# Performance work log

Hardware: AMD Instinct MI355X
Metric: run time of the kernel (lower is better)

Reference implementation:

```python
import jax, jax.numpy as jnp
import numpy as np

# ---- db6 filter bank (pywt conventions) ----
_REC_LO = np.array([0.11154074335008017, 0.4946238903983854, 0.7511339080215775,
                    0.3152503517092432, -0.22626469396516913, -0.12976686756709563,
                    0.09750160558707936, 0.02752286553001629, -0.031582039318031156,
                    0.0005538422009938016, 0.004777257511010651, -0.00107730108499558],
                   dtype=np.float32)
_REC_HI = _REC_LO[::-1].copy(); _REC_HI[1::2] *= -1.0          # qmf(rec_lo)
_DEC_LO = _REC_LO[::-1].copy()
_DEC_HI = _REC_HI[::-1].copy()
L = 12          # filter length
LEVEL = 8       # J
# pytorch_wavelets cross-correlates with dec[::-1] == true conv with dec.
# lax.conv_general_dilated is correlation, so analysis kernels = dec[::-1] = rec filters.
ANA = jnp.asarray(np.stack([_REC_LO, _REC_HI])[:, None, :])     # [2,1,L]
SYN = jnp.asarray(np.stack([_DEC_LO, _DEC_HI])[None, :, :])     # [1,2,L]


def dwt1d(x, J):
    """Multi-level DWT, mode='symmetric'. x: [B,C,N] -> (yl [B,C,m], [yh1..yhJ])."""
    B, C, N = x.shape
    lo = x.reshape(B * C, 1, N)
    highs = []
    for _ in range(J):
        n = lo.shape[-1]
        outlen = (n + L - 1) // 2                    # pywt dwt_coeff_len
        p = 2 * (outlen - 1) - n + L
        xp = jnp.pad(lo, ((0, 0), (0, 0), (p // 2, (p + 1) // 2)), mode='symmetric')
        y = jax.lax.conv_general_dilated(xp, ANA, (2,), 'VALID',
                                         dimension_numbers=('NCH', 'OIH', 'NCH'))
        lo = y[:, :1]
        highs.append(y[:, 1:].reshape(B, C, outlen))
    return lo.reshape(B, C, -1), highs


def idwt1d(yl, yhs):
    """Inverse of dwt1d. yl: [B,C,m], yhs list (level1..levelJ)."""
    B, C, _ = yl.shape
    lo = yl.reshape(B * C, 1, -1)
    pad = L - 1 - (L - 2)                            # torch convT padding L-2 -> lax pad 1
    for h in yhs[::-1]:
        h = h.reshape(B * C, 1, -1)
        if lo.shape[-1] > h.shape[-1]:               # 'unpad' extra sample
            lo = lo[..., :h.shape[-1]]
        xh = jnp.concatenate([lo, h], axis=1)        # [BC,2,n]
        lo = jax.lax.conv_general_dilated(xh, SYN, (1,), [(pad, pad)],
                                          lhs_dilation=(2,),
                                          dimension_numbers=('NCH', 'OIH', 'NCH'))
    return lo.reshape(B, C, -1)


def wno_forward(x, fc0_w, fc0_b, w1, w2, cw, cb, fc1_w, fc1_b, fc2_w, fc2_b):
    B, s, _ = x.shape
    grid = jnp.broadcast_to(jnp.linspace(0.0, 1.0, s, dtype=x.dtype)[None, :, None], (B, s, 1))
    v = jnp.concatenate([x, grid], axis=-1) @ fc0_w + fc0_b     # [B,s,W]
    v = v.transpose(0, 2, 1)                                     # [B,W,s]
    n_layers = w1.shape[0]
    for i in range(n_layers):
        yl, yhs = dwt1d(v, LEVEL)
        yl = jnp.einsum('bix,iox->box', yl, w1[i])               # mix approx coeffs
        yhs[-1] = jnp.einsum('bix,iox->box', yhs[-1], w2[i])     # mix finest-level detail
        x1 = idwt1d(yl, yhs)
        x2 = jnp.einsum('bis,io->bos', v, cw[i]) + cb[i][None, :, None]  # 1x1 conv
        v = x1 + x2
        if i < n_layers - 1:
            v = jax.nn.gelu(v, approximate=False)
    v = v.transpose(0, 2, 1)
    v = jax.nn.gelu(v @ fc1_w + fc1_b, approximate=False)
    return v @ fc2_w + fc2_b                                     # [B,s,1]


def setup_inputs() -> dict:
    key = jax.random.key(0)
    B, S, W, NL = 32, 8192, 64, 4
    n = S
    for _ in range(LEVEL):
        n = (n + L - 1) // 2
    modes = n                                                    # 42
    ks = jax.random.split(key, 12)
    scale = 1.0 / (W * W)
    return {
        'x': jax.random.normal(ks[0], (B, S, 1), jnp.float32),
        'fc0_w': jax.random.normal(ks[1], (2, W), jnp.float32) * 0.5,
        'fc0_b': jax.random.normal(ks[2], (W,), jnp.float32) * 0.1,
        'w1': scale * jax.random.uniform(ks[3], (NL, W, W, modes), jnp.float32),
        'w2': scale * jax.random.uniform(ks[4], (NL, W, W, modes), jnp.float32),
        'cw': jax.random.normal(ks[5], (NL, W, W), jnp.float32) * (1.0 / np.sqrt(W)),
        'cb': jax.random.normal(ks[6], (NL, W), jnp.float32) * 0.05,
        'fc1_w': jax.random.normal(ks[7], (W, 128), jnp.float32) * (1.0 / np.sqrt(W)),
        'fc1_b': jax.random.normal(ks[8], (128,), jnp.float32) * 0.05,
        'fc2_w': jax.random.normal(ks[9], (128, 1), jnp.float32) * (1.0 / np.sqrt(128.0)),
        'fc2_b': jax.random.normal(ks[10], (1,), jnp.float32) * 0.05,
    }


def reference(x, fc0_w, fc0_b, w1, w2, cw, cb, fc1_w, fc1_b, fc2_w, fc2_b):
    return wno_forward(x, fc0_w, fc0_b, w1, w2, cw, cb, fc1_w, fc1_b, fc2_w, fc2_b)
```

## Files before the change

### kernel.cpp

```cpp
#include <hip/hip_runtime.h>
#include <cmath>

#define BC 2048
#define S_LEN 8192
#define MODES 42
#define HTOT 8232

static constexpr float C_LO[12] = {
  0.11154074335008017f, 0.4946238903983854f, 0.7511339080215775f,
  0.3152503517092432f, -0.22626469396516913f, -0.12976686756709563f,
  0.09750160558707936f, 0.02752286553001629f, -0.031582039318031156f,
  0.0005538422009938016f, 0.004777257511010651f, -0.00107730108499558f };

__device__ __forceinline__ float rec_lo_c(int k){ return C_LO[k]; }
__device__ __forceinline__ float rec_hi_c(int k){ float v = C_LO[11-k]; return (k&1)? -v : v; }
__device__ __forceinline__ float dec_lo_c(int k){ return C_LO[11-k]; }
__device__ __forceinline__ float dec_hi_c(int k){ float v = C_LO[k];    return (k&1)?  v : -v; }

__device__ __forceinline__ float erf_fast(float x){
  float ax = fabsf(x);
  float t  = __fdividef(1.0f, 1.0f + 0.3275911f * ax);
  float p  = ((((1.061405429f * t - 1.453152027f) * t) + 1.421413741f) * t - 0.284496736f) * t + 0.254829592f;
  float y  = 1.0f - p * t * __expf(-ax * ax);
  return copysignf(y, x);
}
__device__ __forceinline__ float gelu_f(float x){
  return 0.5f * x * (1.0f + erf_fast(x * 0.70710678118654752440f));
}

__device__ __forceinline__ int reflect_i(int t, int n){
  t = (t < 0) ? (-1 - t) : t;
  t = (t >= n) ? (2 * n - 1 - t) : t;
  return t;
}

__device__ __forceinline__ unsigned short bf16_rn(float x){
  unsigned int b = __float_as_uint(x);
  b += 0x7FFF + ((b >> 16) & 1);
  return (unsigned short)(b >> 16);
}
__device__ __forceinline__ float bf16_to_f(unsigned short h){
  return __uint_as_float(((unsigned int)h) << 16);
}

typedef short  v8s __attribute__((ext_vector_type(8)));
typedef float  v4f __attribute__((ext_vector_type(4)));
typedef unsigned short u16;

__global__ __launch_bounds__(256) void prep_split(
    const float* __restrict__ fc1w, const float* __restrict__ cw,
    u16* __restrict__ whH, u16* __restrict__ whL,
    u16* __restrict__ wcH, u16* __restrict__ wcL)
{
  int i = blockIdx.x * 256 + threadIdx.x;
  if (i < 8192) {
    int c = i >> 7, j = i & 127;
    float wv = fc1w[i];
    u16 h = bf16_rn(wv);
    float lo = wv - bf16_to_f(h);
    int cs = c ^ ((j & 7) << 3);
    whH[j * 64 + cs] = h; whL[j * 64 + cs] = bf16_rn(lo);
  }
  int k = i - 8192;
  if (k >= 0 && k < 16384) {
    int l = k >> 12, r = k & 4095;
    int c = r >> 6, o = r & 63;
    float wv = cw[k];
    u16 h = bf16_rn(wv);
    float lo = wv - bf16_to_f(h);
    int cs = c ^ ((o & 7) << 3);
    wcH[l * 4096 + o * 64 + cs] = h; wcL[l * 4096 + o * 64 + cs] = bf16_rn(lo);
  }
}

__global__ __launch_bounds__(256) void fc0_kernel(
    const float* __restrict__ x, const float* __restrict__ w,
    const float* __restrict__ bias, float* __restrict__ v)
{
  int p = blockIdx.x * 256 + threadIdx.x;
  int b = p >> 13, s = p & 8191;
  float xv = x[p];
  float g  = (float)s * (1.0f / 8191.0f);
  for (int c = 0; c < 64; ++c) {
    v[((size_t)(b * 64 + c)) * S_LEN + s] = xv * w[c] + g * w[64 + c] + bias[c];
  }
}

__global__ __launch_bounds__(256) void dwt_big(
    const float* __restrict__ vin, float* __restrict__ highs, float* __restrict__ lo_f)
{
  __shared__ float sV[2184], sL1[1088], sL2[544];
  int seq = blockIdx.x >> 2, c = blockIdx.x & 3;
  const float* src = vin + (size_t)seq * S_LEN;
  float* hseq = highs + (size_t)seq * HTOT;

  int V0 = 2080 * c - 70;
  for (int i = threadIdx.x; i < 2178; i += 256)
    sV[i] = src[reflect_i(V0 + i, 8192)];
  __syncthreads();

  int base1 = 1040 * c - 30;
  for (int u = threadIdx.x; u < 1082; u += 256) {
    int m1 = base1 + u;
    float alo = 0.f, ahi = 0.f;
    #pragma unroll
    for (int k = 0; k < 12; ++k) {
      float x = sV[2 * m1 + k - 10 - V0];
      alo += x * rec_lo_c(k); ahi += x * rec_hi_c(k);
    }
    sL1[u] = alo;
    if (m1 >= 1040 * c && m1 < 1040 * c + 1040 && m1 >= 0 && m1 < 4101) hseq[m1] = ahi;
  }
  __syncthreads();

  int base2 = 520 * c - 10;
  for (int u = threadIdx.x; u < 534; u += 256) {
    int m2 = base2 + u;
    float alo = 0.f, ahi = 0.f;
    #pragma unroll
    for (int k = 0; k < 12; ++k) {
      int t = reflect_i(2 * m2 + k - 10, 4101);
      float x = sL1[t - base1];
      alo += x * rec_lo_c(k); ahi += x * rec_hi_c(k);
    }
    sL2[u] = alo;
    if (m2 >= 520 * c && m2 < 520 * c + 520 && m2 >= 0 && m2 < 2056) hseq[4101 + m2] = ahi;
  }
  __syncthreads();

  for (int u = threadIdx.x; u < 260; u += 256) {
    int m3 = 260 * c + u;
    if (m3 < 1033) {
      float alo = 0.f, ahi = 0.f;
      #pragma unroll
      for (int k = 0; k < 12; ++k) {
        int t = reflect_i(2 * m3 + k - 10, 2056);
        float x = sL2[t - base2];
        alo += x * rec_lo_c(k); ahi += x * rec_hi_c(k);
      }
      lo_f[(size_t)seq * 1033 + m3] = alo;
      hseq[6157 + m3] = ahi;
    }
  }
}

__device__ __forceinline__ void dwt_lvl(const float* in, int n, float* out, int outn, float* hg)
{
  for (int m = threadIdx.x; m < outn; m += 256) {
    float alo = 0.f, ahi = 0.f;
    #pragma unroll
    for (int k = 0; k < 12; ++k) {
      float x = in[reflect_i(2 * m + k - 10, n)];
      alo += x * rec_lo_c(k); ahi += x * rec_hi_c(k);
    }
    out[m] = alo; hg[m] = ahi;
  }
  __syncthreads();
}

__global__ __launch_bounds__(256) void dwt_small(
    const float* __restrict__ lo_f, float* __restrict__ highs, float* __restrict__ yl)
{
  __shared__ float A[1040], Bb[528];
  int seq = blockIdx.x;
  const float* src = lo_f + (size_t)seq * 1033;
  float* hseq = highs + (size_t)seq * HTOT;
  for (int i = threadIdx.x; i < 1033; i += 256) A[i] = src[i];
  __syncthreads();
  dwt_lvl(A, 1033, Bb, 522, hseq + 7190);
  dwt_lvl(Bb, 522, A, 266, hseq + 7712);
  dwt_lvl(A, 266, Bb, 138, hseq + 7978);
  dwt_lvl(Bb, 138, A, 74, hseq + 8116);
  dwt_lvl(A, 74, Bb, 42, hseq + 8190);
  for (int m = threadIdx.x; m < MODES; m += 256) yl[seq * MODES + m] = Bb[m];
}

__global__ __launch_bounds__(256) void mix2(
    const float* __restrict__ yl_raw, const float* __restrict__ highs,
    const float* __restrict__ w1i, const float* __restrict__ w2i,
    float* __restrict__ yl_m, float* __restrict__ yh_m)
{
  bool hi = blockIdx.x >= 336;
  int idx = (blockIdx.x - (hi ? 336 : 0)) * 256 + threadIdx.x;
  if (idx >= 32 * 64 * MODES) return;
  int xx = idx % MODES;
  int o  = (idx / MODES) % 64;
  int b  = idx / (MODES * 64);
  const float* in = hi ? (highs + 8190) : yl_raw;
  size_t stride   = hi ? HTOT : MODES;
  const float* w  = hi ? w2i : w1i;
  float acc = 0.f;
  for (int i = 0; i < 64; ++i)
    acc += in[((size_t)(b * 64 + i)) * stride + xx] * w[(i * 64 + o) * MODES + xx];
  (hi ? yh_m : yl_m)[(b * 64 + o) * MODES + xx] = acc;
}

__device__ __forceinline__ void idwt_lvl(const float* lo, const float* h, float* out, int outn)
{
  const int par = threadIdx.x & 1;
  for (int m = threadIdx.x; m < outn; m += 256) {
    int t0 = (m - par) >> 1;
    float acc = 0.f;
    #pragma unroll
    for (int i = 0; i < 6; ++i) {
      float cl = par ? dec_lo_c(2 * i) : dec_lo_c(2 * i + 1);
      float ch = par ? dec_hi_c(2 * i) : dec_hi_c(2 * i + 1);
      acc += lo[t0 + i] * cl + h[t0 + i] * ch;
    }
    out[m] = acc;
  }
}

__device__ __forceinline__ void stage_band(float* dst, const float* src, int len, int alloc)
{
  for (int i = threadIdx.x; i < alloc; i += 256) dst[i] = (i < len) ? src[i] : 0.f;
}

__global__ __launch_bounds__(256) void idwt_small(
    const float* __restrict__ yl_m, const float* __restrict__ yh_m,
    const float* __restrict__ highs, float* __restrict__ lo_i)
{
  __shared__ float bands[1132];
  __shared__ float wa[1040], wb[528];
  int seq = blockIdx.x;
  const float* hseq = highs + (size_t)seq * HTOT;
  stage_band(bands + 0,   yl_m + (size_t)seq * MODES, 42, 50);
  stage_band(bands + 50,  yh_m + (size_t)seq * MODES, 42, 50);
  stage_band(bands + 100, hseq + 8116, 74, 82);
  stage_band(bands + 182, hseq + 7978, 138, 146);
  stage_band(bands + 328, hseq + 7712, 266, 274);
  stage_band(bands + 602, hseq + 7190, 522, 530);
  __syncthreads();
  idwt_lvl(bands + 0, bands + 50, wa, 74);    __syncthreads();
  idwt_lvl(wa, bands + 100, wb, 138);         __syncthreads();
  idwt_lvl(wb, bands + 182, wa, 266);         __syncthreads();
  idwt_lvl(wa, bands + 328, wb, 522);         __syncthreads();
  const int par = threadIdx.x & 1;
  for (int m = threadIdx.x; m < 1033; m += 256) {
    int t0 = (m - par) >> 1;
    float acc = 0.f;
    #pragma unroll
    for (int i = 0; i < 6; ++i) {
      float cl = par ? dec_lo_c(2 * i) : dec_lo_c(2 * i + 1);
      float ch = par ? dec_hi_c(2 * i) : dec_hi_c(2 * i + 1);
      acc += wb[t0 + i] * cl + bands[602 + t0 + i] * ch;
    }
    lo_i[(size_t)seq * 1033 + m] = acc;
  }
}

__global__ __launch_bounds__(256) void idwt_big(
    const float* __restrict__ lo_i, const float* __restrict__ highs, float* __restrict__ x1)
{
  __shared__ float sL3[280], sH3[280], sL2[544], sH2[544], sL1[1040], sH1[1040];
  int seq = blockIdx.x >> 2, c = blockIdx.x & 3;
  const float* hseq = highs + (size_t)seq * HTOT;
  const float* l3   = lo_i + (size_t)seq * 1033;
  int b3 = 256 * c - 2, b2 = 512 * c - 2, b1 = 1024 * c - 2;
  const int par = threadIdx.x & 1;

  for (int i = threadIdx.x; i < 280; i += 256) {
    int g = b3 + i;
    bool ok = (g >= 0 && g < 1033);
    sL3[i] = ok ? l3[g] : 0.f;
    sH3[i] = ok ? hseq[6157 + g] : 0.f;
  }
  for (int i = threadIdx.x; i < 536; i += 256) {
    int g = b2 + i;
    sH2[i] = (g >= 0 && g < 2056) ? hseq[4101 + g] : 0.f;
  }
  for (int i = threadIdx.x; i < 1040; i += 256) {
    int g = b1 + i;
    sH1[i] = (g >= 0 && g < 4101) ? hseq[g] : 0.f;
  }
  __syncthreads();

  for (int u = threadIdx.x; u < 536; u += 256) {
    int m = b2 + u;
    int t0 = ((m - par) >> 1) - b3;
    float acc = 0.f;
    #pragma unroll
    for (int i = 0; i < 6; ++i) {
      float cl = par ? dec_lo_c(2 * i) : dec_lo_c(2 * i + 1);
      float ch = par ? dec_hi_c(2 * i) : dec_hi_c(2 * i + 1);
      acc += sL3[t0 + i] * cl + sH3[t0 + i] * ch;
    }
    sL2[u] = (m >= 0 && m < 2056) ? acc : 0.f;
  }
  __syncthreads();

  for (int u = threadIdx.x; u < 1040; u += 256) {
    int m = b1 + u;
    int t0 = ((m - par) >> 1) - b2;
    float acc = 0.f;
    #pragma unroll
    for (int i = 0; i < 6; ++i) {
      float cl = par ? dec_lo_c(2 * i) : dec_lo_c(2 * i + 1);
      float ch = par ? dec_hi_c(2 * i) : dec_hi_c(2 * i + 1);
      acc += sL2[t0 + i] * cl + sH2[t0 + i] * ch;
    }
    sL1[u] = (m >= 0 && m < 4101) ? acc : 0.f;
  }
  __syncthreads();

  for (int u = threadIdx.x; u < 2048; u += 256) {
    int m = 2048 * c + u;
    int t0 = ((m - par) >> 1) - b1;
    float acc = 0.f;
    #pragma unroll
    for (int i = 0; i < 6; ++i) {
      float cl = par ? dec_lo_c(2 * i) : dec_lo_c(2 * i + 1);
      float ch = par ? dec_hi_c(2 * i) : dec_hi_c(2 * i + 1);
      acc += sL1[t0 + i] * cl + sH1[t0 + i] * ch;
    }
    x1[(size_t)seq * S_LEN + m] = acc;
  }
}

__global__ __launch_bounds__(256) void pw_mfma(
    const float* __restrict__ x1, float* v,
    const u16* __restrict__ wcH, const u16* __restrict__ wcL,
    const float* __restrict__ cb, int do_gelu)
{
  __shared__ u16 aH[64][64], aL[64][64];
  __shared__ u16 wH[64][64], wL[64][64];
  __shared__ float cbl[64];
  int b  = blockIdx.x >> 7;
  int s0 = (blockIdx.x & 127) << 6;
  int t  = threadIdx.x;

  {
    const v8s* srcH = (const v8s*)wcH;
    const v8s* srcL = (const v8s*)wcL;
    v8s* dstH = (v8s*)&wH[0][0];
    v8s* dstL = (v8s*)&wL[0][0];
    #pragma unroll
    for (int r = 0; r < 2; ++r) {
      dstH[t + 256 * r] = srcH[t + 256 * r];
      dstL[t + 256 * r] = srcL[t + 256 * r];
    }
  }
  if (t < 64) cbl[t] = cb[t];

  #pragma unroll
  for (int r = 0; r < 4; ++r) {
    int idx = t + 256 * r;
    int ch = idx >> 4, p4 = (idx & 15) << 2;
    float4 xv = *(const float4*)&v[((size_t)(b * 64 + ch)) * S_LEN + s0 + p4];
    u16 h0 = bf16_rn(xv.x); aH[p4+0][ch ^ (((p4+0)&7)<<3)] = h0; aL[p4+0][ch ^ (((p4+0)&7)<<3)] = bf16_rn(xv.x - bf16_to_f(h0));
    u16 h1 = bf16_rn(xv.y); aH[p4+1][ch ^ (((p4+1)&7)<<3)] = h1; aL[p4+1][ch ^ (((p4+1)&7)<<3)] = bf16_rn(xv.y - bf16_to_f(h1));
    u16 h2 = bf16_rn(xv.z); aH[p4+2][ch ^ (((p4+2)&7)<<3)] = h2; aL[p4+2][ch ^ (((p4+2)&7)<<3)] = bf16_rn(xv.z - bf16_to_f(h2));
    u16 h3 = bf16_rn(xv.w); aH[p4+3][ch ^ (((p4+3)&7)<<3)] = h3; aL[p4+3][ch ^ (((p4+3)&7)<<3)] = bf16_rn(xv.w - bf16_to_f(h3));
  }
  __syncthreads();

  int l = t & 63, wv_ = t >> 6;
  int pi = l & 15, kg = l >> 4;
  int pos = wv_ * 16 + pi;
  int swz = (pi & 7) << 3;

  v4f acc[4];
  #pragma unroll
  for (int i = 0; i < 4; ++i) acc[i] = v4f{0.f, 0.f, 0.f, 0.f};

  #pragma unroll
  for (int kt = 0; kt < 2; ++kt) {
    int ka = (kg * 8 + kt * 32) ^ swz;
    v8s ah = *(const v8s*)&aH[pos][ka];
    v8s al = *(const v8s*)&aL[pos][ka];
    #pragma unroll
    for (int ct = 0; ct < 4; ++ct) {
      int o = ct * 16 + pi;
      v8s bh = *(const v8s*)&wH[o][ka];
      v8s bl = *(const v8s*)&wL[o][ka];
      acc[ct] = __builtin_amdgcn_mfma_f32_16x16x32_bf16(ah, bh, acc[ct], 0, 0, 0);
      acc[ct] = __builtin_amdgcn_mfma_f32_16x16x32_bf16(ah, bl, acc[ct], 0, 0, 0);
      acc[ct] = __builtin_amdgcn_mfma_f32_16x16x32_bf16(al, bh, acc[ct], 0, 0, 0);
    }
  }

  #pragma unroll
  for (int ct = 0; ct < 4; ++ct) {
    int o = ct * 16 + pi;
    size_t base = ((size_t)(b * 64 + o)) * S_LEN + s0 + wv_ * 16 + kg * 4;
    float4 x4 = *(const float4*)&x1[base];
    float cbv = cbl[o];
    float y0 = acc[ct][0] + x4.x + cbv;
    float y1 = acc[ct][1] + x4.y + cbv;
    float y2 = acc[ct][2] + x4.z + cbv;
    float y3 = acc[ct][3] + x4.w + cbv;
    if (do_gelu) { y0 = gelu_f(y0); y1 = gelu_f(y1); y2 = gelu_f(y2); y3 = gelu_f(y3); }
    float4 y4 = make_float4(y0, y1, y2, y3);
    *(float4*)&v[base] = y4;
  }
}

__global__ __launch_bounds__(256) void head_mfma(
    const float* __restrict__ v,
    const u16* __restrict__ whH, const u16* __restrict__ whL,
    const float* __restrict__ fc1b, const float* __restrict__ fc2w,
    const float* __restrict__ fc2b, float* __restrict__ out)
{
  __shared__ u16 aH[64][64], aL[64][64];
  __shared__ u16 wH[128][64], wL[128][64];
  __shared__ float f1b[128], f2w[128];
  int b  = blockIdx.x >> 7;
  int s0 = (blockIdx.x & 127) << 6;
  int t  = threadIdx.x;

  {
    const v8s* srcH = (const v8s*)whH;
    const v8s* srcL = (const v8s*)whL;
    v8s* dstH = (v8s*)&wH[0][0];
    v8s* dstL = (v8s*)&wL[0][0];
    #pragma unroll
    for (int r = 0; r < 4; ++r) {
      dstH[t + 256 * r] = srcH[t + 256 * r];
      dstL[t + 256 * r] = srcL[t + 256 * r];
    }
  }
  if (t < 128) { f1b[t] = fc1b[t]; f2w[t] = fc2w[t]; }

  #pragma unroll
  for (int r = 0; r < 4; ++r) {
    int idx = t + 256 * r;
    int ch = idx >> 4, p4 = (idx & 15) << 2;
    float4 xv = *(const float4*)&v[((size_t)(b * 64 + ch)) * S_LEN + s0 + p4];
    u16 h0 = bf16_rn(xv.x); aH[p4+0][ch ^ (((p4+0)&7)<<3)] = h0; aL[p4+0][ch ^ (((p4+0)&7)<<3)] = bf16_rn(xv.x - bf16_to_f(h0));
    u16 h1 = bf16_rn(xv.y); aH[p4+1][ch ^ (((p4+1)&7)<<3)] = h1; aL[p4+1][ch ^ (((p4+1)&7)<<3)] = bf16_rn(xv.y - bf16_to_f(h1));
    u16 h2 = bf16_rn(xv.z); aH[p4+2][ch ^ (((p4+2)&7)<<3)] = h2; aL[p4+2][ch ^ (((p4+2)&7)<<3)] = bf16_rn(xv.z - bf16_to_f(h2));
    u16 h3 = bf16_rn(xv.w); aH[p4+3][ch ^ (((p4+3)&7)<<3)] = h3; aL[p4+3][ch ^ (((p4+3)&7)<<3)] = bf16_rn(xv.w - bf16_to_f(h3));
  }
  __syncthreads();

  int l = t & 63, wv_ = t >> 6;
  int pi = l & 15, kg = l >> 4;
  int pos = wv_ * 16 + pi;
  int swz = (pi & 7) << 3;

  v4f acc[8];
  #pragma unroll
  for (int i = 0; i < 8; ++i) acc[i] = v4f{0.f, 0.f, 0.f, 0.f};

  #pragma unroll
  for (int kt = 0; kt < 2; ++kt) {
    int ka = (kg * 8 + kt * 32) ^ swz;
    v8s ah = *(const v8s*)&aH[pos][ka];
    v8s al = *(const v8s*)&aL[pos][ka];
    #pragma unroll
    for (int ct = 0; ct < 8; ++ct) {
      int j = ct * 16 + pi;
      v8s bh = *(const v8s*)&wH[j][ka];
      v8s bl = *(const v8s*)&wL[j][ka];
      acc[ct] = __builtin_amdgcn_mfma_f32_16x16x32_bf16(ah, bh, acc[ct], 0, 0, 0);
      acc[ct] = __builtin_amdgcn_mfma_f32_16x16x32_bf16(ah, bl, acc[ct], 0, 0, 0);
      acc[ct] = __builtin_amdgcn_mfma_f32_16x16x32_bf16(al, bh, acc[ct], 0, 0, 0);
    }
  }

  float part[4] = {0.f, 0.f, 0.f, 0.f};
  #pragma unroll
  for (int ct = 0; ct < 8; ++ct) {
    int j = ct * 16 + pi;
    float bias = f1b[j], f2 = f2w[j];
    #pragma unroll
    for (int r = 0; r < 4; ++r) {
      float d = acc[ct][r] + bias;
      part[r] += f2 * gelu_f(d);
    }
  }
  #pragma unroll
  for (int r = 0; r < 4; ++r) {
    part[r] += __shfl_xor(part[r], 1, 16);
    part[r] += __shfl_xor(part[r], 2, 16);
    part[r] += __shfl_xor(part[r], 4, 16);
    part[r] += __shfl_xor(part[r], 8, 16);
  }
  if (pi == 0) {
    float b2 = fc2b[0];
    float4 o4 = make_float4(part[0] + b2, part[1] + b2, part[2] + b2, part[3] + b2);
    *(float4*)&out[(size_t)b * S_LEN + s0 + wv_ * 16 + kg * 4] = o4;
  }
}

extern "C" void kernel_launch(void* const* d_in, const int* in_sizes, int n_in,
                              void* d_out, int out_size, void* d_ws, size_t ws_size,
                              hipStream_t stream) {
  const float* x    = (const float*)d_in[0];
  const float* fc0w = (const float*)d_in[1];
  const float* fc0b = (const float*)d_in[2];
  const float* w1   = (const float*)d_in[3];
  const float* w2   = (const float*)d_in[4];
  const float* cw   = (const float*)d_in[5];
  const float* cb   = (const float*)d_in[6];
  const float* fc1w = (const float*)d_in[7];
  const float* fc1b = (const float*)d_in[8];
  const float* fc2w = (const float*)d_in[9];
  const float* fc2b = (const float*)d_in[10];
  float* out = (float*)d_out;

  float* ws     = (float*)d_ws;
  float* v      = ws;
  float* x1     = v      + (size_t)BC * S_LEN;
  float* highs  = x1     + (size_t)BC * S_LEN;
  float* yl_raw = highs  + (size_t)BC * HTOT;
  float* yl_m   = yl_raw + (size_t)BC * MODES;
  float* yh_m   = yl_m   + (size_t)BC * MODES;
  float* lo_f   = yh_m   + (size_t)BC * MODES;
  float* lo_i   = lo_f   + (size_t)BC * 1033;
  u16*   whH    = (u16*)(lo_i + (size_t)BC * 1033);
  u16*   whL    = whH + 8192;
  u16*   wcH    = whL + 8192;
  u16*   wcL    = wcH + 16384;
  size_t needed = (size_t)((char*)(wcL + 16384) - (char*)ws);
  if (ws_size < needed) return;

  prep_split<<<96, 256, 0, stream>>>(fc1w, cw, whH, whL, wcH, wcL);
  fc0_kernel<<<1024, 256, 0, stream>>>(x, fc0w, fc0b, v);

  for (int i = 0; i < 4; ++i) {
    dwt_big<<<BC * 4, 256, 0, stream>>>(v, highs, lo_f);
    dwt_small<<<BC, 256, 0, stream>>>(lo_f, highs, yl_raw);
    mix2<<<672, 256, 0, stream>>>(yl_raw, highs, w1 + (size_t)i * 64 * 64 * MODES,
                                  w2 + (size_t)i * 64 * 64 * MODES, yl_m, yh_m);
    idwt_small<<<BC, 256, 0, stream>>>(yl_m, yh_m, highs, lo_i);
    idwt_big<<<BC * 4, 256, 0, stream>>>(lo_i, highs, x1);
    pw_mfma<<<4096, 256, 0, stream>>>(x1, v, wcH + i * 4096, wcL + i * 4096, cb + i * 64, (i < 3) ? 1 : 0);
  }

  head_mfma<<<4096, 256, 0, stream>>>(v, whH, whL, fc1b, fc2w, fc2b, out);
}
```

Before: 641.3 us.

## Vectorize wavelet transform kernels with float4 loads and aligned band layout

Rewrites the forward and inverse wavelet kernels so each thread computes 4 or 8 adjacent outputs from a register window filled by float4 loads from shared memory. Global staging and stores also become float4. The high-band storage is re-padded to 16-byte-aligned offsets, the low-band buffer gets a padded stride, and boundary reflection is applied as a post-pass instead of per-tap reflect_i index math. This cuts per-tap index arithmetic and scalar shared/global memory traffic, at the cost of more registers per thread and fewer active threads per level.

```diff
diff --git a/kernel.cpp b/kernel.cpp
--- a/kernel.cpp
+++ b/kernel.cpp
@@ -4,7 +4,8 @@
 #define BC 2048
 #define S_LEN 8192
 #define MODES 42
-#define HTOT 8232
+#define HTOT 8248
+#define LO_STR 1036
 
 static constexpr float C_LO[12] = {
   0.11154074335008017f, 0.4946238903983854f, 0.7511339080215775f,
@@ -46,6 +47,48 @@
 typedef short  v8s __attribute__((ext_vector_type(8)));
 typedef float  v4f __attribute__((ext_vector_type(4)));
 typedef unsigned short u16;
+
+__device__ __forceinline__ void ld3f4(float* w, const float* s){
+  *(float4*)&w[0] = *(const float4*)&s[0];
+  *(float4*)&w[4] = *(const float4*)&s[4];
+  *(float4*)&w[8] = *(const float4*)&s[8];
+}
+__device__ __forceinline__ void ld5f4(float* w, const float* s){
+  *(float4*)&w[0]  = *(const float4*)&s[0];
+  *(float4*)&w[4]  = *(const float4*)&s[4];
+  *(float4*)&w[8]  = *(const float4*)&s[8];
+  *(float4*)&w[12] = *(const float4*)&s[12];
+  *(float4*)&w[16] = *(const float4*)&s[16];
+}
+
+__device__ __forceinline__ void stage_g(float* dst, const float* src, int g0, int cnt, int n){
+  for (int j4 = threadIdx.x; j4 < (cnt >> 2); j4 += 256) {
+    int g = g0 + 4 * j4;
+    float4 val;
+    if (g >= 0 && g + 3 < n) val = *(const float4*)&src[g];
+    else {
+      val.x = (g   >= 0 && g   < n) ? src[g]   : 0.f;
+      val.y = (g+1 >= 0 && g+1 < n) ? src[g+1] : 0.f;
+      val.z = (g+2 >= 0 && g+2 < n) ? src[g+2] : 0.f;
+      val.w = (g+3 >= 0 && g+3 < n) ? src[g+3] : 0.f;
+    }
+    *(float4*)&dst[4*j4] = val;
+  }
+}
+
+template<int OFF>
+__device__ __forceinline__ float idwt_tap(const float* wl, const float* wh, int d){
+  float acc = 0.f;
+  int t = OFF + (d >> 1);
+  if (d & 1) {
+    #pragma unroll
+    for (int i = 0; i < 6; ++i) acc += wl[t+i]*dec_lo_c(2*i)   + wh[t+i]*dec_hi_c(2*i);
+  } else {
+    #pragma unroll
+    for (int i = 0; i < 6; ++i) acc += wl[t+i]*dec_lo_c(2*i+1) + wh[t+i]*dec_hi_c(2*i+1);
+  }
+  return acc;
+}
 
 __global__ __launch_bounds__(256) void prep_split(
     const float* __restrict__ fc1w, const float* __restrict__ cw,
@@ -89,71 +132,125 @@
 __global__ __launch_bounds__(256) void dwt_big(
     const float* __restrict__ vin, float* __restrict__ highs, float* __restrict__ lo_f)
 {
-  __shared__ float sV[2184], sL1[1088], sL2[544];
+  __shared__ alignas(16) float sV[2184], sL1[1088], sL2[544];
   int seq = blockIdx.x >> 2, c = blockIdx.x & 3;
   const float* src = vin + (size_t)seq * S_LEN;
   float* hseq = highs + (size_t)seq * HTOT;
-
-  int V0 = 2080 * c - 70;
-  for (int i = threadIdx.x; i < 2178; i += 256)
-    sV[i] = src[reflect_i(V0 + i, 8192)];
+  int tid = threadIdx.x;
+
+  int g0 = 2080 * c - 72;
+  for (int j4 = tid; j4 < 545; j4 += 256) {
+    int g = g0 + 4 * j4;
+    float4 val;
+    if (g >= 0 && g + 3 < 8192) val = *(const float4*)&src[g];
+    else {
+      val.x = src[reflect_i(g,   8192)];
+      val.y = src[reflect_i(g+1, 8192)];
+      val.z = src[reflect_i(g+2, 8192)];
+      val.w = src[reflect_i(g+3, 8192)];
+    }
+    *(float4*)&sV[4*j4] = val;
+  }
   __syncthreads();
 
   int base1 = 1040 * c - 30;
-  for (int u = threadIdx.x; u < 1082; u += 256) {
-    int m1 = base1 + u;
-    float alo = 0.f, ahi = 0.f;
-    #pragma unroll
-    for (int k = 0; k < 12; ++k) {
-      float x = sV[2 * m1 + k - 10 - V0];
-      alo += x * rec_lo_c(k); ahi += x * rec_hi_c(k);
-    }
-    sL1[u] = alo;
-    if (m1 >= 1040 * c && m1 < 1040 * c + 1040 && m1 >= 0 && m1 < 4101) hseq[m1] = ahi;
-  }
+  for (int u0 = 4*tid; u0 < 1082; u0 += 1024) {
+    float w[20];
+    ld5f4(w, &sV[2*u0]);
+    #pragma unroll
+    for (int d = 0; d < 4; ++d) {
+      if (u0 + d < 1082) {
+        float alo = 0.f, ahi = 0.f;
+        #pragma unroll
+        for (int k = 0; k < 12; ++k) {
+          float x = w[2*d + 2 + k];
+          alo += x * rec_lo_c(k); ahi += x * rec_hi_c(k);
+        }
+        sL1[u0+d] = alo;
+        int m1 = base1 + u0 + d;
+        if (m1 >= 1040*c && m1 < 1040*c + 1040 && m1 >= 0 && m1 < 4101) hseq[m1] = ahi;
+      }
+    }
+  }
+  __syncthreads();
+  if (c == 0) { for (int u = tid;        u < 30;   u += 256) sL1[u] = sL1[59 - u]; }
+  if (c == 3) { for (int u = 1011 + tid; u < 1082; u += 256) sL1[u] = sL1[2021 - u]; }
   __syncthreads();
 
   int base2 = 520 * c - 10;
-  for (int u = threadIdx.x; u < 534; u += 256) {
-    int m2 = base2 + u;
-    float alo = 0.f, ahi = 0.f;
-    #pragma unroll
-    for (int k = 0; k < 12; ++k) {
-      int t = reflect_i(2 * m2 + k - 10, 4101);
-      float x = sL1[t - base1];
-      alo += x * rec_lo_c(k); ahi += x * rec_hi_c(k);
-    }
-    sL2[u] = alo;
-    if (m2 >= 520 * c && m2 < 520 * c + 520 && m2 >= 0 && m2 < 2056) hseq[4101 + m2] = ahi;
-  }
-  __syncthreads();
-
-  for (int u = threadIdx.x; u < 260; u += 256) {
-    int m3 = 260 * c + u;
-    if (m3 < 1033) {
-      float alo = 0.f, ahi = 0.f;
+  for (int u0 = 4*tid; u0 < 534; u0 += 1024) {
+    float w[20];
+    ld5f4(w, &sL1[2*u0]);
+    #pragma unroll
+    for (int d = 0; d < 4; ++d) {
+      if (u0 + d < 534) {
+        float alo = 0.f, ahi = 0.f;
+        #pragma unroll
+        for (int k = 0; k < 12; ++k) {
+          float x = w[2*d + k];
+          alo += x * rec_lo_c(k); ahi += x * rec_hi_c(k);
+        }
+        sL2[u0+d] = alo;
+        int m2 = base2 + u0 + d;
+        if (m2 >= 520*c && m2 < 520*c + 520 && m2 >= 0 && m2 < 2056) hseq[4104 + m2] = ahi;
+      }
+    }
+  }
+  __syncthreads();
+  if (c == 0) { for (int u = tid;       u < 10;  u += 256) sL2[u] = sL2[19 - u]; }
+  if (c == 3) { for (int u = 506 + tid; u < 534; u += 256) sL2[u] = sL2[1011 - u]; }
+  __syncthreads();
+
+  for (int u0 = 4*tid; u0 < 260; u0 += 1024) {
+    float w[20];
+    ld5f4(w, &sL2[2*u0]);
+    #pragma unroll
+    for (int d = 0; d < 4; ++d) {
+      int m3 = 260*c + u0 + d;
+      if (u0 + d < 260 && m3 < 1033) {
+        float alo = 0.f, ahi = 0.f;
+        #pragma unroll
+        for (int k = 0; k < 12; ++k) {
+          float x = w[2*d + k];
+          alo += x * rec_lo_c(k); ahi += x * rec_hi_c(k);
+        }
+        lo_f[(size_t)seq * LO_STR + m3] = alo;
+        hseq[6160 + m3] = ahi;
+      }
+    }
+  }
+}
+
+__device__ __forceinline__ void dwt_lvl_v(const float* in, int n, float* out, int outn, float* hg)
+{
+  for (int u0 = 4*(int)threadIdx.x; u0 < outn; u0 += 1024) {
+    bool fast = (u0 >= 8) && (2*u0 + 7 < n) && (u0 + 3 < outn);
+    if (fast) {
+      float w[20];
+      ld5f4(w, &in[2*u0 - 12]);
       #pragma unroll
-      for (int k = 0; k < 12; ++k) {
-        int t = reflect_i(2 * m3 + k - 10, 2056);
-        float x = sL2[t - base2];
-        alo += x * rec_lo_c(k); ahi += x * rec_hi_c(k);
+      for (int d = 0; d < 4; ++d) {
+        float alo = 0.f, ahi = 0.f;
+        #pragma unroll
+        for (int k = 0; k < 12; ++k) {
+          float x = w[2*d + 2 + k];
+          alo += x * rec_lo_c(k); ahi += x * rec_hi_c(k);
+        }
+        out[u0+d] = alo; hg[u0+d] = ahi;
       }
-      lo_f[(size_t)seq * 1033 + m3] = alo;
-      hseq[6157 + m3] = ahi;
-    }
-  }
-}
-
-__device__ __forceinline__ void dwt_lvl(const float* in, int n, float* out, int outn, float* hg)
-{
-  for (int m = threadIdx.x; m < outn; m += 256) {
-    float alo = 0.f, ahi = 0.f;
-    #pragma unroll
-    for (int k = 0; k < 12; ++k) {
-      float x = in[reflect_i(2 * m + k - 10, n)];
-      alo += x * rec_lo_c(k); ahi += x * rec_hi_c(k);
-    }
-    out[m] = alo; hg[m] = ahi;
+    } else {
+      for (int d = 0; d < 4; ++d) {
+        if (u0 + d < outn) {
+          float alo = 0.f, ahi = 0.f;
+          #pragma unroll
+          for (int k = 0; k < 12; ++k) {
+            float x = in[reflect_i(2*(u0+d) + k - 10, n)];
+            alo += x * rec_lo_c(k); ahi += x * rec_hi_c(k);
+          }
+          out[u0+d] = alo; hg[u0+d] = ahi;
+        }
+      }
+    }
   }
   __syncthreads();
 }
@@ -161,17 +258,20 @@
 __global__ __launch_bounds__(256) void dwt_small(
     const float* __restrict__ lo_f, float* __restrict__ highs, float* __restrict__ yl)
 {
-  __shared__ float A[1040], Bb[528];
+  __shared__ alignas(16) float A[1040], Bb[528];
   int seq = blockIdx.x;
-  const float* src = lo_f + (size_t)seq * 1033;
+  const float* src = lo_f + (size_t)seq * LO_STR;
   float* hseq = highs + (size_t)seq * HTOT;
-  for (int i = threadIdx.x; i < 1033; i += 256) A[i] = src[i];
-  __syncthreads();
-  dwt_lvl(A, 1033, Bb, 522, hseq + 7190);
-  dwt_lvl(Bb, 522, A, 266, hseq + 7712);
-  dwt_lvl(A, 266, Bb, 138, hseq + 7978);
-  dwt_lvl(Bb, 138, A, 74, hseq + 8116);
-  dwt_lvl(A, 74, Bb, 42, hseq + 8190);
+  for (int i = 4*(int)threadIdx.x; i < 1033; i += 1024) {
+    if (i + 3 < 1033) *(float4*)&A[i] = *(const float4*)&src[i];
+    else { for (int d = 0; d < 4; ++d) if (i + d < 1033) A[i+d] = src[i+d]; }
+  }
+  __syncthreads();
+  dwt_lvl_v(A, 1033, Bb, 522, hseq + 7196);
+  dwt_lvl_v(Bb, 522, A, 266, hseq + 7720);
+  dwt_lvl_v(A, 266, Bb, 138, hseq + 7988);
+  dwt_lvl_v(Bb, 138, A, 74,  hseq + 8128);
+  dwt_lvl_v(A, 74,  Bb, 42,  hseq + 8204);
   for (int m = threadIdx.x; m < MODES; m += 256) yl[seq * MODES + m] = Bb[m];
 }
 
@@ -186,7 +286,7 @@
   int xx = idx % MODES;
   int o  = (idx / MODES) % 64;
   int b  = idx / (MODES * 64);
-  const float* in = hi ? (highs + 8190) : yl_raw;
+  const float* in = hi ? (highs + 8204) : yl_raw;
   size_t stride   = hi ? HTOT : MODES;
   const float* w  = hi ? w2i : w1i;
   float acc = 0.f;
@@ -195,20 +295,17 @@
   (hi ? yh_m : yl_m)[(b * 64 + o) * MODES + xx] = acc;
 }
 
-__device__ __forceinline__ void idwt_lvl(const float* lo, const float* h, float* out, int outn)
-{
-  const int par = threadIdx.x & 1;
-  for (int m = threadIdx.x; m < outn; m += 256) {
-    int t0 = (m - par) >> 1;
-    float acc = 0.f;
-    #pragma unroll
-    for (int i = 0; i < 6; ++i) {
-      float cl = par ? dec_lo_c(2 * i) : dec_lo_c(2 * i + 1);
-      float ch = par ? dec_hi_c(2 * i) : dec_hi_c(2 * i + 1);
-      acc += lo[t0 + i] * cl + h[t0 + i] * ch;
-    }
-    out[m] = acc;
-  }
+__device__ __forceinline__ void idwt_lvl8(const float* lo, const float* h, float* out, int outn)
+{
+  for (int u0 = 8*(int)threadIdx.x; u0 < outn; u0 += 2048) {
+    int ib = u0 >> 1;
+    float wl[12], wh[12];
+    ld3f4(wl, &lo[ib]); ld3f4(wh, &h[ib]);
+    #pragma unroll
+    for (int d = 0; d < 8; ++d)
+      if (u0 + d < outn) out[u0+d] = idwt_tap<0>(wl, wh, d);
+  }
+  __syncthreads();
 }
 
 __device__ __forceinline__ void stage_band(float* dst, const float* src, int len, int alloc)
@@ -220,100 +317,93 @@
     const float* __restrict__ yl_m, const float* __restrict__ yh_m,
     const float* __restrict__ highs, float* __restrict__ lo_i)
 {
-  __shared__ float bands[1132];
-  __shared__ float wa[1040], wb[528];
+  __shared__ alignas(16) float bands[1120], wa[272], wb[528];
   int seq = blockIdx.x;
   const float* hseq = highs + (size_t)seq * HTOT;
-  stage_band(bands + 0,   yl_m + (size_t)seq * MODES, 42, 50);
-  stage_band(bands + 50,  yh_m + (size_t)seq * MODES, 42, 50);
-  stage_band(bands + 100, hseq + 8116, 74, 82);
-  stage_band(bands + 182, hseq + 7978, 138, 146);
-  stage_band(bands + 328, hseq + 7712, 266, 274);
-  stage_band(bands + 602, hseq + 7190, 522, 530);
-  __syncthreads();
-  idwt_lvl(bands + 0, bands + 50, wa, 74);    __syncthreads();
-  idwt_lvl(wa, bands + 100, wb, 138);         __syncthreads();
-  idwt_lvl(wb, bands + 182, wa, 266);         __syncthreads();
-  idwt_lvl(wa, bands + 328, wb, 522);         __syncthreads();
-  const int par = threadIdx.x & 1;
-  for (int m = threadIdx.x; m < 1033; m += 256) {
-    int t0 = (m - par) >> 1;
-    float acc = 0.f;
-    #pragma unroll
-    for (int i = 0; i < 6; ++i) {
-      float cl = par ? dec_lo_c(2 * i) : dec_lo_c(2 * i + 1);
-      float ch = par ? dec_hi_c(2 * i) : dec_hi_c(2 * i + 1);
-      acc += wb[t0 + i] * cl + bands[602 + t0 + i] * ch;
-    }
-    lo_i[(size_t)seq * 1033 + m] = acc;
+  stage_band(bands + 0,   yl_m + (size_t)seq * MODES, 42, 48);
+  stage_band(bands + 48,  yh_m + (size_t)seq * MODES, 42, 48);
+  stage_band(bands + 96,  hseq + 8128, 74, 80);
+  stage_band(bands + 176, hseq + 7988, 138, 144);
+  stage_band(bands + 320, hseq + 7720, 266, 272);
+  stage_band(bands + 592, hseq + 7196, 522, 528);
+  __syncthreads();
+  idwt_lvl8(bands + 0,  bands + 48,  wa, 74);
+  idwt_lvl8(wa,         bands + 96,  wb, 138);
+  idwt_lvl8(wb,         bands + 176, wa, 266);
+  idwt_lvl8(wa,         bands + 320, wb, 522);
+  for (int u0 = 8*(int)threadIdx.x; u0 < 1033; u0 += 2048) {
+    int ib = u0 >> 1;
+    float wl[12], wh[12];
+    ld3f4(wl, &wb[ib]); ld3f4(wh, &bands[592 + ib]);
+    float o[8];
+    #pragma unroll
+    for (int d = 0; d < 8; ++d) o[d] = idwt_tap<0>(wl, wh, d);
+    float* dst = lo_i + (size_t)seq * LO_STR + u0;
+    if (u0 + 7 < 1033) {
+      *(float4*)&dst[0] = make_float4(o[0], o[1], o[2], o[3]);
+      *(float4*)&dst[4] = make_float4(o[4], o[5], o[6], o[7]);
+    } else {
+      for (int d = 0; d < 8; ++d) if (u0 + d < 1033) dst[d] = o[d];
+    }
   }
 }
 
 __global__ __launch_bounds__(256) void idwt_big(
     const float* __restrict__ lo_i, const float* __restrict__ highs, float* __restrict__ x1)
 {
-  __shared__ float sL3[280], sH3[280], sL2[544], sH2[544], sL1[1040], sH1[1040];
+  __shared__ alignas(16) float sL3[288], sH3[288], sL2[544], sH2[544], sL1[1048], sH1[1048];
   int seq = blockIdx.x >> 2, c = blockIdx.x & 3;
   const float* hseq = highs + (size_t)seq * HTOT;
-  const float* l3   = lo_i + (size_t)seq * 1033;
-  int b3 = 256 * c - 2, b2 = 512 * c - 2, b1 = 1024 * c - 2;
-  const int par = threadIdx.x & 1;
-
-  for (int i = threadIdx.x; i < 280; i += 256) {
-    int g = b3 + i;
-    bool ok = (g >= 0 && g < 1033);
-    sL3[i] = ok ? l3[g] : 0.f;
-    sH3[i] = ok ? hseq[6157 + g] : 0.f;
-  }
-  for (int i = threadIdx.x; i < 536; i += 256) {
-    int g = b2 + i;
-    sH2[i] = (g >= 0 && g < 2056) ? hseq[4101 + g] : 0.f;
-  }
-  for (int i = threadIdx.x; i < 1040; i += 256) {
-    int g = b1 + i;
-    sH1[i] = (g >= 0 && g < 4101) ? hseq[g] : 0.f;
-  }
-  __syncthreads();
-
-  for (int u = threadIdx.x; u < 536; u += 256) {
-    int m = b2 + u;
-    int t0 = ((m - par) >> 1) - b3;
-    float acc = 0.f;
-    #pragma unroll
-    for (int i = 0; i < 6; ++i) {
-      float cl = par ? dec_lo_c(2 * i) : dec_lo_c(2 * i + 1);
-      float ch = par ? dec_hi_c(2 * i) : dec_hi_c(2 * i + 1);
-      acc += sL3[t0 + i] * cl + sH3[t0 + i] * ch;
-    }
-    sL2[u] = (m >= 0 && m < 2056) ? acc : 0.f;
-  }
-  __syncthreads();
-
-  for (int u = threadIdx.x; u < 1040; u += 256) {
-    int m = b1 + u;
-    int t0 = ((m - par) >> 1) - b2;
-    float acc = 0.f;
-    #pragma unroll
-    for (int i = 0; i < 6; ++i) {
-      float cl = par ? dec_lo_c(2 * i) : dec_lo_c(2 * i + 1);
-      float ch = par ? dec_hi_c(2 * i) : dec_hi_c(2 * i + 1);
-      acc += sL2[t0 + i] * cl + sH2[t0 + i] * ch;
-    }
-    sL1[u] = (m >= 0 && m < 4101) ? acc : 0.f;
-  }
-  __syncthreads();
-
-  for (int u = threadIdx.x; u < 2048; u += 256) {
-    int m = 2048 * c + u;
-    int t0 = ((m - par) >> 1) - b1;
-    float acc = 0.f;
-    #pragma unroll
-    for (int i = 0; i < 6; ++i) {
-      float cl = par ? dec_lo_c(2 * i) : dec_lo_c(2 * i + 1);
-      float ch = par ? dec_hi_c(2 * i) : dec_hi_c(2 * i + 1);
-      acc += sL1[t0 + i] * cl + sH1[t0 + i] * ch;
-    }
-    x1[(size_t)seq * S_LEN + m] = acc;
+  const float* l3   = lo_i + (size_t)seq * LO_STR;
+  int g3 = 256*c - 4, g2 = 512*c - 4, g1 = 1024*c - 4;
+
+  stage_g(sL3, l3,          g3, 288, 1033);
+  stage_g(sH3, hseq + 6160, g3, 288, 1033);
+  stage_g(sH2, hseq + 4104, g2, 544, 2056);
+  stage_g(sH1, hseq,        g1, 1048, 4101);
+  __syncthreads();
+
+  for (int u0 = 8*(int)threadIdx.x; u0 < 536; u0 += 2048) {
+    int ib = u0 >> 1;
+    float wl[12], wh[12];
+    ld3f4(wl, &sL3[ib]); ld3f4(wh, &sH3[ib]);
+    #pragma unroll
+    for (int d = 0; d < 8; ++d) {
+      if (u0 + d < 536) {
+        int m = 512*c - 2 + u0 + d;
+        float acc = idwt_tap<3>(wl, wh, d);
+        sL2[u0 + d + 2] = (m >= 0 && m < 2056) ? acc : 0.f;
+      }
+    }
+  }
+  __syncthreads();
+
+  for (int u0 = 8*(int)threadIdx.x; u0 < 1040; u0 += 2048) {
+    int ib = u0 >> 1;
+    float wl[12], wh[12];
+    ld3f4(wl, &sL2[ib]); ld3f4(wh, &sH2[ib]);
+    #pragma unroll
+    for (int d = 0; d < 8; ++d) {
+      if (u0 + d < 1040) {
+        int m = 1024*c - 2 + u0 + d;
+        float acc = idwt_tap<3>(wl, wh, d);
+        sL1[u0 + d + 2] = (m >= 0 && m < 4101) ? acc : 0.f;
+      }
+    }
+  }
+  __syncthreads();
+
+  {
+    int u0 = 8*(int)threadIdx.x;
+    int ib = (u0 >> 1) + 4;
+    float wl[12], wh[12];
+    ld3f4(wl, &sL1[ib]); ld3f4(wh, &sH1[ib]);
+    float o[8];
+    #pragma unroll
+    for (int d = 0; d < 8; ++d) o[d] = idwt_tap<0>(wl, wh, d);
+    float* dst = x1 + (size_t)seq * S_LEN + 2048*c + u0;
+    *(float4*)&dst[0] = make_float4(o[0], o[1], o[2], o[3]);
+    *(float4*)&dst[4] = make_float4(o[4], o[5], o[6], o[7]);
   }
 }
 
@@ -507,8 +597,8 @@
   float* yl_m   = yl_raw + (size_t)BC * MODES;
   float* yh_m   = yl_m   + (size_t)BC * MODES;
   float* lo_f   = yh_m   + (size_t)BC * MODES;
-  float* lo_i   = lo_f   + (size_t)BC * 1033;
-  u16*   whH    = (u16*)(lo_i + (size_t)BC * 1033);
+  float* lo_i   = lo_f   + (size_t)BC * LO_STR;
+  u16*   whH    = (u16*)(lo_i + (size_t)BC * LO_STR);
   u16*   whL    = whH + 8192;
   u16*   wcH    = whL + 8192;
   u16*   wcL    = wcH + 16384;
```

After: 610.1 us. 4.9% less time.
